# Kernel tuning notes

Measured on AMD Instinct MI355X. Metric: run time of the kernel, lower is better.

## Reference

```python
import jax, jax.numpy as jnp
import numpy as np

D = 768
H = 16
DH = D // H  # 48


def setup_inputs() -> dict:
    key = jax.random.key(0)
    ks = jax.random.split(key, 7)
    s = 0.02
    x = jax.random.normal(ks[0], (4, 2048, D), dtype=jnp.float32)
    # weights stored as (in, out); torch Linear is y = x @ W.T + b
    W_qkv = jax.random.normal(ks[1], (D, 3 * D), dtype=jnp.float32) * s
    b_qkv = jax.random.normal(ks[2], (3 * D,), dtype=jnp.float32) * s
    W_o = jax.random.normal(ks[3], (D, D), dtype=jnp.float32) * s
    b_o = jax.random.normal(ks[4], (D,), dtype=jnp.float32) * s
    W_p = jax.random.normal(ks[5], (D, D), dtype=jnp.float32) * s
    b_p = jax.random.normal(ks[6], (D,), dtype=jnp.float32) * s
    return {"x": x, "W_qkv": W_qkv, "b_qkv": b_qkv, "W_o": W_o, "b_o": b_o, "W_p": W_p, "b_p": b_p}


def reference(x, W_qkv, b_qkv, W_o, b_o, W_p, b_p):
    b, n, _ = x.shape
    qkv = x @ W_qkv + b_qkv                     # (b, n, 3*D)
    # reshape to (b, n, H, 3*DH) as in torch, then chunk last dim into q,k,v
    # -> per-head interleaved layout [q_h | k_h | v_h]
    qkv = qkv.reshape(b, n, H, 3, DH).transpose(0, 2, 1, 3, 4)  # (b, H, n, 3, DH)
    q, k, v = qkv[..., 0, :], qkv[..., 1, :], qkv[..., 2, :]    # (b, H, n, DH)
    alpha = jnp.einsum("bhqd,bhkd->bhqk", q, k) / jnp.sqrt(jnp.float32(DH))
    alpha = jax.nn.softmax(alpha, axis=-1)      # dropout: eval mode (identity)
    out = jnp.einsum("bhqk,bhkd->bhqd", alpha, v)
    out = out.transpose(0, 2, 1, 3).reshape(b, n, D)
    out = out @ W_o + b_o
    out = out @ W_p + b_p
    return out
```

## Files before the change

### kernel.cpp

```cpp
#include <hip/hip_runtime.h>

#define DEV __device__ __forceinline__

typedef __attribute__((ext_vector_type(4))) float f32x4;
typedef __attribute__((ext_vector_type(8))) short bf16x8;
typedef __attribute__((ext_vector_type(4))) short bf16x4;
typedef __attribute__((ext_vector_type(4))) unsigned int u32x4;

DEV short f2bf(float f) {
  union { float f; unsigned u; } c; c.f = f;
  unsigned r = c.u + 0x7FFFu + ((c.u >> 16) & 1u);
  return (short)(r >> 16);
}

DEV unsigned cvtpk(float lo, float hi) {
  unsigned r;
  asm("v_cvt_pk_bf16_f32 %0, %1, %2" : "=v"(r) : "v"(lo), "v"(hi));
  return r;
}

DEV float exp2r(float x) { return __builtin_amdgcn_exp2f(x); }

DEV void gl_lds16(short* lds, const short* g) {
  __builtin_amdgcn_global_load_lds(
      (__attribute__((address_space(1))) void*)(void*)g,
      (__attribute__((address_space(3))) void*)lds, 16, 0, 0);
}

__global__ __launch_bounds__(256) void k_cvt(const float* __restrict__ in, short* __restrict__ out) {
  int i = blockIdx.x * 256 + threadIdx.x;
  float4 v = reinterpret_cast<const float4*>(in)[i];
  bf16x4 o;
  o[0] = f2bf(v.x); o[1] = f2bf(v.y); o[2] = f2bf(v.z); o[3] = f2bf(v.w);
  reinterpret_cast<bf16x4*>(out)[i] = o;
}

__global__ __launch_bounds__(256) void k_tcvt(const float* __restrict__ W, short* __restrict__ WT,
                                              int Kd, int Nd) {
  __shared__ float t[32][33];
  int nb = blockIdx.x * 32, kb = blockIdx.y * 32;
  int tx = threadIdx.x, ty = threadIdx.y;
#pragma unroll
  for (int i = ty; i < 32; i += 8) t[i][tx] = W[(long)(kb + i) * Nd + nb + tx];
  __syncthreads();
#pragma unroll
  for (int i = ty; i < 32; i += 8) WT[(long)(nb + i) * Kd + kb + tx] = f2bf(t[tx][i]);
}

__global__ __launch_bounds__(256) void k_bias(const float* __restrict__ bo, const float* __restrict__ bp,
                                              const float* __restrict__ Wp, float* __restrict__ bc) {
  int j = blockIdx.x * 256 + threadIdx.x;
  int k0 = blockIdx.y * 48;
  float s = 0.f;
#pragma unroll
  for (int k = 0; k < 48; ++k) s += bo[k0 + k] * Wp[(long)(k0 + k) * 768 + j];
  if (blockIdx.y == 0) s += bp[j];
  atomicAdd(&bc[j], s);
}

template <int MODE>
__global__ __launch_bounds__(256) void k_gemm(
    const short* __restrict__ A, const short* __restrict__ BT, const float* __restrict__ bias,
    short* __restrict__ Cb, float* __restrict__ Cf,
    short* __restrict__ Qp, short* __restrict__ Kp, short* __restrict__ VT,
    int M, int N, int K) {
  __shared__ short As[128 * 32];
  __shared__ short Bs[128 * 32];
  const int tid = threadIdx.x;
  const int w = tid >> 6, lane = tid & 63;
  const int lr = lane & 15, g = lane >> 4;
  const int m0 = blockIdx.y * 128, n0 = blockIdx.x * 128;
  const int wm = (w >> 1) * 64, wn = (w & 1) * 64;

  f32x4 acc[4][4];
#pragma unroll
  for (int i = 0; i < 4; ++i)
#pragma unroll
    for (int j = 0; j < 4; ++j)
#pragma unroll
      for (int r = 0; r < 4; ++r) acc[i][j][r] = 0.f;

  const short* Ab = A + (long)m0 * K;
  const short* Bb = BT + (long)n0 * K;
  const int row_s = tid >> 2;
  const int c_s = tid & 3;
  const int nk = K >> 5;

  for (int kt = 0; kt < nk; ++kt) {
    const int k0 = kt << 5;
#pragma unroll
    for (int i = 0; i < 2; ++i) {
      int row = row_s + i * 64;
      int cs = c_s ^ ((row >> 1) & 3);
      gl_lds16(As + (i * 256 + w * 64) * 8, Ab + (long)row * K + k0 + cs * 8);
      gl_lds16(Bs + (i * 256 + w * 64) * 8, Bb + (long)row * K + k0 + cs * 8);
    }
    __syncthreads();
    bf16x8 af[4], bf[4];
#pragma unroll
    for (int mi = 0; mi < 4; ++mi) {
      int r = wm + mi * 16 + lr;
      int c = g ^ ((r >> 1) & 3);
      af[mi] = *reinterpret_cast<const bf16x8*>(As + r * 32 + c * 8);
    }
#pragma unroll
    for (int nj = 0; nj < 4; ++nj) {
      int r = wn + nj * 16 + lr;
      int c = g ^ ((r >> 1) & 3);
      bf[nj] = *reinterpret_cast<const bf16x8*>(Bs + r * 32 + c * 8);
    }
#pragma unroll
    for (int mi = 0; mi < 4; ++mi)
#pragma unroll
      for (int nj = 0; nj < 4; ++nj)
        acc[mi][nj] = __builtin_amdgcn_mfma_f32_16x16x32_bf16(af[mi], bf[nj], acc[mi][nj], 0, 0, 0);
    __syncthreads();
  }

#pragma unroll
  for (int nj = 0; nj < 4; ++nj) {
    int col = n0 + wn + nj * 16 + lr;
    float bv = (MODE == 3) ? 0.f : bias[col];
    if (MODE == 0) {
      int h = col / 144;
      int rem = col - h * 144;
      int s = rem / 48;
      int d = rem - s * 48;
#pragma unroll
      for (int mi = 0; mi < 4; ++mi)
#pragma unroll
        for (int r = 0; r < 4; ++r) {
          int row = m0 + wm + mi * 16 + g * 4 + r;
          float val = acc[mi][nj][r] + bv;
          int b = row >> 11, n = row & 2047;
          int bh = (b << 4) + h;
          if (s == 0) {
            long o = ((long)(bh * 2048 + n)) * 64 + d;
            Qp[o] = f2bf(val * 0.20823051649867783f);
            if (d < 16) Qp[o + 48] = 0;
          } else if (s == 1) {
            long o = ((long)(bh * 2048 + n)) * 64 + d;
            Kp[o] = f2bf(val);
            if (d < 16) Kp[o + 48] = 0;
          } else {
            VT[((long)(bh * 48 + d)) * 2048 + n] = f2bf(val);
          }
        }
    } else {
#pragma unroll
      for (int mi = 0; mi < 4; ++mi)
#pragma unroll
        for (int r = 0; r < 4; ++r) {
          int row = m0 + wm + mi * 16 + g * 4 + r;
          float val = acc[mi][nj][r] + bv;
          if (MODE == 2) Cf[(long)row * N + col] = val;
          else           Cb[(long)row * N + col] = f2bf(val);
        }
    }
  }
}

__global__ __launch_bounds__(256, 4) void k_attn(const short* __restrict__ Q, const short* __restrict__ K,
                                                 const short* __restrict__ VT, short* __restrict__ AO) {
  const int tid = threadIdx.x, w = tid >> 6, lane = tid & 63;
  const int lr = lane & 15, g = lane >> 4;
  const int orig = blockIdx.x;
  const int logical = (orig & 7) * 128 + (orig >> 3);
  const int bh = logical >> 4;
  const int q0 = (logical & 15) * 128 + w * 32;

  const short* Qh = Q + (long)bh * 2048 * 64;
  const short* Kh = K + (long)bh * 2048 * 64;
  const short* VTh = VT + (long)bh * 48 * 2048;

  __shared__ short Ks[2][64 * 64];
  __shared__ short Vs[2][48 * 64];

  const int r_l = lane >> 3, c_l = lane & 7;
  const int gc8 = (c_l ^ r_l) * 8;

  bf16x8 bq0 = *reinterpret_cast<const bf16x8*>(Qh + (q0 + lr) * 64 + g * 8);
  bf16x8 bq1 = *reinterpret_cast<const bf16x8*>(Qh + (q0 + lr) * 64 + 32 + g * 8);
  bf16x8 bq2 = *reinterpret_cast<const bf16x8*>(Qh + (q0 + 16 + lr) * 64 + g * 8);
  bf16x8 bq3 = *reinterpret_cast<const bf16x8*>(Qh + (q0 + 16 + lr) * 64 + 32 + g * 8);

  bf16x8 vones;
#pragma unroll
  for (int i = 0; i < 8; ++i) vones[i] = (short)0x3F80;

  f32x4 accA[3], accB[3];
#pragma unroll
  for (int df = 0; df < 3; ++df)
#pragma unroll
    for (int r = 0; r < 4; ++r) { accA[df][r] = 0.f; accB[df][r] = 0.f; }
  f32x4 acclA = {0.f, 0.f, 0.f, 0.f}, acclB = {0.f, 0.f, 0.f, 0.f};

  const short* kg = Kh + (long)(w * 8 + r_l) * 64 + gc8;
  const short* vg = VTh + (long)(w * 8 + r_l) * 2048 + gc8;

  auto STAGE = [&](int b) {
    gl_lds16(&Ks[b][w * 512], kg);
    gl_lds16(&Ks[b][(w + 4) * 512], kg + 2048);
    gl_lds16(&Vs[b][w * 512], vg);
    if (w < 2) gl_lds16(&Vs[b][(w + 4) * 512], vg + 65536);
  };

  STAGE(0);
  kg += 4096; vg += 64;
  asm volatile("s_waitcnt vmcnt(0)" ::: "memory");
  __syncthreads();

  const int sw = lr & 7;
  const int goff = (g & 1) * 4;
  const int ghalf = g >> 1;

  for (int t = 0; t < 32; ++t) {
    const int cur = t & 1;
    if (t < 31) {
      STAGE(cur ^ 1);
      kg += 4096; vg += 64;
    }

    const short* KsC = Ks[cur];
    const short* VsC = Vs[cur];

    f32x4 stA[4], stB[4];
    __builtin_amdgcn_s_setprio(1);
#pragma unroll
    for (int kf = 0; kf < 4; ++kf) {
      const short* kr = KsC + (kf * 16 + lr) * 64;
      bf16x8 a0 = *reinterpret_cast<const bf16x8*>(kr + (g ^ sw) * 8);
      bf16x8 a1 = *reinterpret_cast<const bf16x8*>(kr + ((4 + g) ^ sw) * 8);
      f32x4 sA = {0.f, 0.f, 0.f, 0.f}, sB = {0.f, 0.f, 0.f, 0.f};
      sA = __builtin_amdgcn_mfma_f32_16x16x32_bf16(a0, bq0, sA, 0, 0, 0);
      sB = __builtin_amdgcn_mfma_f32_16x16x32_bf16(a0, bq2, sB, 0, 0, 0);
      sA = __builtin_amdgcn_mfma_f32_16x16x32_bf16(a1, bq1, sA, 0, 0, 0);
      sB = __builtin_amdgcn_mfma_f32_16x16x32_bf16(a1, bq3, sB, 0, 0, 0);
      stA[kf] = sA; stB[kf] = sB;
    }
    __builtin_amdgcn_s_setprio(0);

#pragma unroll
    for (int kf = 0; kf < 4; ++kf)
#pragma unroll
      for (int r = 0; r < 4; ++r) {
        stA[kf][r] = exp2r(stA[kf][r]);
        stB[kf][r] = exp2r(stB[kf][r]);
      }

    __builtin_amdgcn_s_setprio(1);
#pragma unroll
    for (int ks = 0; ks < 2; ++ks) {
      u32x4 bwA, bwB;
      bwA[0] = cvtpk(stA[2 * ks][0], stA[2 * ks][1]);
      bwA[1] = cvtpk(stA[2 * ks][2], stA[2 * ks][3]);
      bwA[2] = cvtpk(stA[2 * ks + 1][0], stA[2 * ks + 1][1]);
      bwA[3] = cvtpk(stA[2 * ks + 1][2], stA[2 * ks + 1][3]);
      bwB[0] = cvtpk(stB[2 * ks][0], stB[2 * ks][1]);
      bwB[1] = cvtpk(stB[2 * ks][2], stB[2 * ks][3]);
      bwB[2] = cvtpk(stB[2 * ks + 1][0], stB[2 * ks + 1][1]);
      bwB[3] = cvtpk(stB[2 * ks + 1][2], stB[2 * ks + 1][3]);
      bf16x8 bpA = __builtin_bit_cast(bf16x8, bwA);
      bf16x8 bpB = __builtin_bit_cast(bf16x8, bwB);
      const int off_lo = ((ks * 4 + ghalf) ^ sw) * 8 + goff;
      const int off_hi = ((ks * 4 + 2 + ghalf) ^ sw) * 8 + goff;
      acclA = __builtin_amdgcn_mfma_f32_16x16x32_bf16(vones, bpA, acclA, 0, 0, 0);
      acclB = __builtin_amdgcn_mfma_f32_16x16x32_bf16(vones, bpB, acclB, 0, 0, 0);
#pragma unroll
      for (int df = 0; df < 3; ++df) {
        const short* vbase = VsC + (df * 16 + lr) * 64;
        union { bf16x8 v; bf16x4 h[2]; } av;
        av.h[0] = *reinterpret_cast<const bf16x4*>(vbase + off_lo);
        av.h[1] = *reinterpret_cast<const bf16x4*>(vbase + off_hi);
        accA[df] = __builtin_amdgcn_mfma_f32_16x16x32_bf16(av.v, bpA, accA[df], 0, 0, 0);
        accB[df] = __builtin_amdgcn_mfma_f32_16x16x32_bf16(av.v, bpB, accB[df], 0, 0, 0);
      }
    }
    __builtin_amdgcn_s_setprio(0);

    asm volatile("s_waitcnt vmcnt(0)" ::: "memory");
    __syncthreads();
  }

  int b = bh >> 4, h = bh & 15;
  float invA = 1.f / acclA[0];
  float invB = 1.f / acclB[0];
  long rowA = ((long)((b << 11) + q0 + lr)) * 768 + h * 48;
  long rowB = ((long)((b << 11) + q0 + 16 + lr)) * 768 + h * 48;
#pragma unroll
  for (int df = 0; df < 3; ++df) {
    bf16x4 oA, oB;
#pragma unroll
    for (int r = 0; r < 4; ++r) { oA[r] = f2bf(accA[df][r] * invA); oB[r] = f2bf(accB[df][r] * invB); }
    *reinterpret_cast<bf16x4*>(AO + rowA + df * 16 + g * 4) = oA;
    *reinterpret_cast<bf16x4*>(AO + rowB + df * 16 + g * 4) = oB;
  }
}

extern "C" void kernel_launch(void* const* d_in, const int* in_sizes, int n_in,
                              void* d_out, int out_size, void* d_ws, size_t ws_size,
                              hipStream_t stream) {
  const float* x    = (const float*)d_in[0];
  const float* Wqkv = (const float*)d_in[1];
  const float* bqkv = (const float*)d_in[2];
  const float* Wo   = (const float*)d_in[3];
  const float* bo   = (const float*)d_in[4];
  const float* Wp   = (const float*)d_in[5];
  const float* bp   = (const float*)d_in[6];

  char* ws = (char*)d_ws;
  short* xb    = (short*)(ws + 0);
  short* WqkvT = (short*)(ws + 12582912);
  short* WpT   = (short*)(ws + 17301504);
  short* Qp    = (short*)(ws + 18481152);
  short* Kp    = (short*)(ws + 35258368);
  short* VT    = (short*)(ws + 52035584);
  short* AO    = (short*)(ws + 64618496);
  short* Wob   = (short*)(ws + 0);
  short* WoWpT = (short*)(ws + 2097152);
  float* bc    = (float*)(ws + 4194304);

  k_cvt<<<6144, 256, 0, stream>>>(x, xb);
  k_tcvt<<<dim3(72, 24), dim3(32, 8), 0, stream>>>(Wqkv, WqkvT, 768, 2304);
  k_tcvt<<<dim3(24, 24), dim3(32, 8), 0, stream>>>(Wp, WpT, 768, 768);

  k_gemm<0><<<dim3(18, 64), 256, 0, stream>>>(xb, WqkvT, bqkv, nullptr, nullptr,
                                              Qp, Kp, VT, 8192, 2304, 768);
  k_cvt<<<576, 256, 0, stream>>>(Wo, Wob);
  k_gemm<3><<<dim3(6, 6), 256, 0, stream>>>(WpT, Wob, nullptr, WoWpT, nullptr,
                                            nullptr, nullptr, nullptr, 768, 768, 768);
  hipMemsetAsync(bc, 0, 768 * sizeof(float), stream);
  k_bias<<<dim3(3, 16), 256, 0, stream>>>(bo, bp, Wp, bc);

  k_attn<<<1024, 256, 0, stream>>>(Qp, Kp, VT, AO);
  k_gemm<2><<<dim3(6, 64), 256, 0, stream>>>(AO, WoWpT, bc, nullptr, (float*)d_out,
                                             nullptr, nullptr, nullptr, 8192, 768, 768);
}
```

Measured before the change: 193.0 us.

## Double-buffer GEMM LDS tiles, remap blocks across XCDs, raise MFMA priority

The GEMM kernel now keeps two LDS stages and issues the next K-tile's global-to-LDS loads before running MFMAs on the current tile, so memory latency can overlap compute. This replaces the old load-then-barrier pattern. Block indices are remapped so consecutive tiles land on the same XCD for better L2 locality, and the MFMA section runs at raised wave priority. The cost is double the LDS footprint per block, which may reduce occupancy.

```diff
diff --git a/kernel.cpp b/kernel.cpp
--- a/kernel.cpp
+++ b/kernel.cpp
@@ -25,6 +25,12 @@
   __builtin_amdgcn_global_load_lds(
       (__attribute__((address_space(1))) void*)(void*)g,
       (__attribute__((address_space(3))) void*)lds, 16, 0, 0);
+}
+
+DEV int xcd_swz(int orig, int nwg) {
+  int q = nwg >> 3, r = nwg & 7;
+  int xcd = orig & 7, idx = orig >> 3;
+  return (xcd < r ? xcd * (q + 1) : r * (q + 1) + (xcd - r) * q) + idx;
 }
 
 __global__ __launch_bounds__(256) void k_cvt(const float* __restrict__ in, short* __restrict__ out) {
@@ -64,12 +70,17 @@
     short* __restrict__ Cb, float* __restrict__ Cf,
     short* __restrict__ Qp, short* __restrict__ Kp, short* __restrict__ VT,
     int M, int N, int K) {
-  __shared__ short As[128 * 32];
-  __shared__ short Bs[128 * 32];
+  __shared__ short As[2][128 * 32];
+  __shared__ short Bs[2][128 * 32];
   const int tid = threadIdx.x;
   const int w = tid >> 6, lane = tid & 63;
   const int lr = lane & 15, g = lane >> 4;
-  const int m0 = blockIdx.y * 128, n0 = blockIdx.x * 128;
+
+  const int nbx = gridDim.x;
+  int lin = blockIdx.y * nbx + blockIdx.x;
+  lin = xcd_swz(lin, nbx * gridDim.y);
+  const int bx = lin % nbx, by = lin / nbx;
+  const int m0 = by * 128, n0 = bx * 128;
   const int wm = (w >> 1) * 64, wn = (w & 1) * 64;
 
   f32x4 acc[4][4];
@@ -86,34 +97,48 @@
   const int c_s = tid & 3;
   const int nk = K >> 5;
 
-  for (int kt = 0; kt < nk; ++kt) {
-    const int k0 = kt << 5;
+  auto STAGE = [&](int b, int k0) {
 #pragma unroll
     for (int i = 0; i < 2; ++i) {
       int row = row_s + i * 64;
       int cs = c_s ^ ((row >> 1) & 3);
-      gl_lds16(As + (i * 256 + w * 64) * 8, Ab + (long)row * K + k0 + cs * 8);
-      gl_lds16(Bs + (i * 256 + w * 64) * 8, Bb + (long)row * K + k0 + cs * 8);
-    }
-    __syncthreads();
+      gl_lds16(&As[b][(i * 256 + w * 64) * 8], Ab + (long)row * K + k0 + cs * 8);
+      gl_lds16(&Bs[b][(i * 256 + w * 64) * 8], Bb + (long)row * K + k0 + cs * 8);
+    }
+  };
+
+  STAGE(0, 0);
+  asm volatile("s_waitcnt vmcnt(0)" ::: "memory");
+  __syncthreads();
+
+  for (int kt = 0; kt < nk; ++kt) {
+    const int cur = kt & 1;
+    if (kt + 1 < nk) STAGE(cur ^ 1, (kt + 1) << 5);
+
+    const short* AsC = As[cur];
+    const short* BsC = Bs[cur];
     bf16x8 af[4], bf[4];
 #pragma unroll
     for (int mi = 0; mi < 4; ++mi) {
       int r = wm + mi * 16 + lr;
       int c = g ^ ((r >> 1) & 3);
-      af[mi] = *reinterpret_cast<const bf16x8*>(As + r * 32 + c * 8);
+      af[mi] = *reinterpret_cast<const bf16x8*>(AsC + r * 32 + c * 8);
     }
 #pragma unroll
     for (int nj = 0; nj < 4; ++nj) {
       int r = wn + nj * 16 + lr;
       int c = g ^ ((r >> 1) & 3);
-      bf[nj] = *reinterpret_cast<const bf16x8*>(Bs + r * 32 + c * 8);
-    }
+      bf[nj] = *reinterpret_cast<const bf16x8*>(BsC + r * 32 + c * 8);
+    }
+    __builtin_amdgcn_s_setprio(1);
 #pragma unroll
     for (int mi = 0; mi < 4; ++mi)
 #pragma unroll
       for (int nj = 0; nj < 4; ++nj)
         acc[mi][nj] = __builtin_amdgcn_mfma_f32_16x16x32_bf16(af[mi], bf[nj], acc[mi][nj], 0, 0, 0);
+    __builtin_amdgcn_s_setprio(0);
+
+    asm volatile("s_waitcnt vmcnt(0)" ::: "memory");
     __syncthreads();
   }
 
```

New measurement: 184.2 us. 1.05x faster.
